# Optimization experiments

Measured on AMD Instinct MI355X. Metric: run time of the kernel, lower is better.

The kernel has to match this reference:

```python
import jax, jax.numpy as jnp
import numpy as np

N = 50000        # nodes
E = 1600000      # edges (avg degree 32)
F_IN = 512       # input features
HID = 8          # hidden per head (hardcoded in module)
HEADS = 8        # in_head (hardcoded in module)
CLS = 16         # num_classes
NEG_SLOPE = 0.2  # PyG GATConv default


def setup_inputs() -> dict:
    key = jax.random.key(0)
    ks = jax.random.split(key, 12)
    s = 0.05
    return {
        "x": jax.random.normal(ks[0], (N, F_IN), dtype=jnp.float32),
        "edge_index": jax.random.randint(ks[1], (2, E), 0, N, dtype=jnp.int64),
        "W1": jax.random.normal(ks[2], (F_IN, HEADS * HID), dtype=jnp.float32) * s,
        "att_src1": jax.random.normal(ks[3], (HEADS, HID), dtype=jnp.float32) * s,
        "att_dst1": jax.random.normal(ks[4], (HEADS, HID), dtype=jnp.float32) * s,
        "bias1": jax.random.normal(ks[5], (HEADS * HID,), dtype=jnp.float32) * s,
        "W2": jax.random.normal(ks[6], (HEADS * HID, CLS), dtype=jnp.float32) * s,
        "att_src2": jax.random.normal(ks[7], (1, CLS), dtype=jnp.float32) * s,
        "att_dst2": jax.random.normal(ks[8], (1, CLS), dtype=jnp.float32) * s,
        "bias2": jax.random.normal(ks[9], (CLS,), dtype=jnp.float32) * s,
    }


def _gat_conv(x, src, dst, W, att_src, att_dst, bias, n, heads, ch, concat):
    # Linear projection: [n, heads, ch]
    h = (x @ W).reshape(n, heads, ch)
    # Per-node attention logits (PyG style): alpha_src/dst = sum(h * a)
    a_src = jnp.einsum("nhc,hc->nh", h, att_src)  # [n, heads]
    a_dst = jnp.einsum("nhc,hc->nh", h, att_dst)
    # Per-edge raw score, leaky_relu, then segment softmax over incoming edges per dst
    e = jax.nn.leaky_relu(a_src[src] + a_dst[dst], NEG_SLOPE)  # [Etot, heads]
    m = jax.ops.segment_max(e, dst, num_segments=n)            # [n, heads]
    w = jnp.exp(e - m[dst])
    den = jax.ops.segment_sum(w, dst, num_segments=n)
    alpha = w / den[dst]                                        # [Etot, heads]
    # Scatter-aggregate weighted source features
    out = jax.ops.segment_sum(h[src] * alpha[..., None], dst, num_segments=n)  # [n, heads, ch]
    out = out.reshape(n, heads * ch) if concat else out.mean(axis=1)
    return out + bias


def reference(x, edge_index, W1, att_src1, att_dst1, bias1, W2, att_src2, att_dst2, bias2):
    n = x.shape[0]
    # PyG GATConv adds self-loops by default
    loops = jnp.arange(n, dtype=edge_index.dtype)
    src = jnp.concatenate([edge_index[0], loops])
    dst = jnp.concatenate([edge_index[1], loops])
    # dropout(p=0.6) is identity in eval mode
    h = _gat_conv(x, src, dst, W1, att_src1, att_dst1, bias1, n, HEADS, HID, True)
    h = jax.nn.elu(h)
    out = _gat_conv(h, src, dst, W2, att_src2, att_dst2, bias2, n, 1, CLS, False)
    return jax.nn.log_softmax(out, axis=1)
```

## Files before the change

### kernel.cpp

```cpp
#include <hip/hip_runtime.h>
#include <cstddef>

#define N_NODES 50000
#define N_EDGES 1600000
#define N_ETOT  (N_EDGES + N_NODES)
#define F_IN    512
#define HEADS   8
#define HID     8
#define CLS     16

#define NBUCK   196
#define BCAP    12288
#define CHUNKA  4096

typedef float v4 __attribute__((ext_vector_type(4)));
typedef float v2 __attribute__((ext_vector_type(2)));
typedef unsigned short us4 __attribute__((ext_vector_type(4)));
typedef unsigned int u4 __attribute__((ext_vector_type(4)));

__device__ inline float b2f_lo(unsigned int u) { return __uint_as_float(u << 16); }
__device__ inline float b2f_hi(unsigned int u) { return __uint_as_float(u & 0xffff0000u); }
__device__ inline unsigned short f2b(float f) {
  unsigned int x = __float_as_uint(f);
  unsigned int r = (x + 0x7fffu + ((x >> 16) & 1u)) >> 16;
  return (unsigned short)r;
}

__global__ __launch_bounds__(256) void gemm1_kernel(
    const float* __restrict__ x, const float* __restrict__ W,
    const float* __restrict__ att_src, const float* __restrict__ att_dst,
    unsigned short* __restrict__ h1b, float* __restrict__ a_src,
    float* __restrict__ a_dst, int nrows) {
  __shared__ float xs[64][36];
  __shared__ float ws[32][68];
  int t  = threadIdx.x;
  int tx = t & 15, ty = t >> 4;
  int row0 = blockIdx.x * 64;
  v4 acc[4];
  acc[0] = 0.f; acc[1] = 0.f; acc[2] = 0.f; acc[3] = 0.f;

  for (int k0 = 0; k0 < F_IN; k0 += 32) {
#pragma unroll
    for (int r = 0; r < 2; ++r) {
      int idx = t + r * 256;
      int m = idx >> 3;
      int kk = (idx & 7) * 4;
      v4 v = 0.f;
      int grow = row0 + m;
      if (grow < nrows) v = *(const v4*)(x + (size_t)grow * F_IN + k0 + kk);
      *(v4*)&xs[m][kk] = v;
    }
#pragma unroll
    for (int r = 0; r < 2; ++r) {
      int idx = t + r * 256;
      int kk = idx >> 4;
      int nn = (idx & 15) * 4;
      *(v4*)&ws[kk][nn] = *(const v4*)(W + (size_t)(k0 + kk) * 64 + nn);
    }
    __syncthreads();
#pragma unroll
    for (int kk = 0; kk < 32; kk += 4) {
      v4 a[4], b[4];
#pragma unroll
      for (int i = 0; i < 4; ++i) a[i] = *(const v4*)&xs[ty * 4 + i][kk];
#pragma unroll
      for (int tt = 0; tt < 4; ++tt) b[tt] = *(const v4*)&ws[kk + tt][tx * 4];
#pragma unroll
      for (int i = 0; i < 4; ++i) {
        acc[i] += a[i][0] * b[0];
        acc[i] += a[i][1] * b[1];
        acc[i] += a[i][2] * b[2];
        acc[i] += a[i][3] * b[3];
      }
    }
    __syncthreads();
  }
  v4 avs = *(const v4*)(att_src + tx * 4);
  v4 avd = *(const v4*)(att_dst + tx * 4);
#pragma unroll
  for (int i = 0; i < 4; ++i) {
    int grow = row0 + ty * 4 + i;
    float ps = acc[i][0]*avs[0] + acc[i][1]*avs[1] + acc[i][2]*avs[2] + acc[i][3]*avs[3];
    float pd = acc[i][0]*avd[0] + acc[i][1]*avd[1] + acc[i][2]*avd[2] + acc[i][3]*avd[3];
    ps += __shfl_xor(ps, 1);
    pd += __shfl_xor(pd, 1);
    if (grow < nrows) {
      us4 o;
      o.x = f2b(acc[i][0]); o.y = f2b(acc[i][1]);
      o.z = f2b(acc[i][2]); o.w = f2b(acc[i][3]);
      *(us4*)(h1b + (size_t)grow * 64 + tx * 4) = o;
      if (!(tx & 1)) {
        int head = tx >> 1;
        a_src[grow * 8 + head] = ps;
        a_dst[grow * 8 + head] = pd;
      }
    }
  }
}

__global__ __launch_bounds__(256) void bucketA_kernel(
    const int* __restrict__ src_idx, const int* __restrict__ dst_idx,
    int* __restrict__ gcur, int* __restrict__ abuck) {
  __shared__ int hist[NBUCK];
  __shared__ int base[NBUCK];
  __shared__ int cur[NBUCK];
  int t = threadIdx.x;
  if (t < NBUCK) hist[t] = 0;
  __syncthreads();
  int e0 = blockIdx.x * CHUNKA;
  int eend = e0 + CHUNKA;
  if (eend > N_EDGES) eend = N_EDGES;
  for (int e = e0 + t; e < eend; e += 256)
    atomicAdd(&hist[(unsigned)dst_idx[e] >> 8], 1);
  __syncthreads();
  if (t < NBUCK) {
    int c = hist[t];
    base[t] = c ? atomicAdd(&gcur[t], c) : 0;
    cur[t] = 0;
  }
  __syncthreads();
  for (int e = e0 + t; e < eend; e += 256) {
    int s = src_idx[e];
    int d = dst_idx[e];
    int b = (unsigned)d >> 8;
    int r = atomicAdd(&cur[b], 1);
    abuck[b * BCAP + base[b] + r] = (s << 8) | (d & 255);
  }
}

__global__ __launch_bounds__(256) void bucket_scan_kernel(
    const int* __restrict__ gcur, int* __restrict__ bucket_base,
    int* __restrict__ indptr) {
  __shared__ int sm[256];
  int t = threadIdx.x;
  int nnodes = N_NODES - t * 256;
  if (nnodes > 256) nnodes = 256;
  if (nnodes < 0) nnodes = 0;
  int v = (t < NBUCK) ? gcur[t] + nnodes : 0;
  sm[t] = v;
  __syncthreads();
  for (int o = 1; o < 256; o <<= 1) {
    int u = (t >= o) ? sm[t - o] : 0;
    __syncthreads();
    sm[t] += u;
    __syncthreads();
  }
  if (t < NBUCK) bucket_base[t] = sm[t] - v;
  if (t == 0) indptr[N_NODES] = N_ETOT;
}

__global__ __launch_bounds__(256) void bucketB_kernel(
    const int* __restrict__ gcur, const int* __restrict__ bucket_base,
    const int* __restrict__ abuck, int* __restrict__ indptr,
    int* __restrict__ csr_src) {
  __shared__ int hist[256];
  __shared__ int sm[256];
  __shared__ int cur[256];
  int b = blockIdx.x;
  int t = threadIdx.x;
  int M = gcur[b];
  int node0 = b * 256;
  int nnodes = N_NODES - node0;
  if (nnodes > 256) nnodes = 256;
  hist[t] = (t < nnodes) ? 1 : 0;
  __syncthreads();
  const int* ab = abuck + b * BCAP;
  for (int i = t; i < M; i += 256)
    atomicAdd(&hist[ab[i] & 255], 1);
  __syncthreads();
  int v = hist[t];
  sm[t] = v;
  __syncthreads();
  for (int o = 1; o < 256; o <<= 1) {
    int u = (t >= o) ? sm[t - o] : 0;
    __syncthreads();
    sm[t] += u;
    __syncthreads();
  }
  int bbase = bucket_base[b];
  int excl = sm[t] - v;
  cur[t] = excl;
  if (t < nnodes) indptr[node0 + t] = bbase + excl;
  __syncthreads();
  for (int i = t; i < M; i += 256) {
    int entry = ab[i];
    int r = atomicAdd(&cur[entry & 255], 1);
    csr_src[bbase + r] = entry >> 8;
  }
  if (t < nnodes) {
    int r = atomicAdd(&cur[t], 1);
    csr_src[bbase + r] = node0 + t;
  }
}

__global__ __launch_bounds__(256) void agg1_kernel(
    const int* __restrict__ indptr, const int* __restrict__ csr_src,
    const unsigned short* __restrict__ h1b, const float* __restrict__ a_src1,
    const float* __restrict__ a_dst1, const float* __restrict__ bias1,
    float* __restrict__ h_elu, int n) {
  int wave = threadIdx.x >> 6;
  int lane = threadIdx.x & 63;
  int node = blockIdx.x * 4 + wave;
  if (node >= n) return;
  int j = lane >> 3;
  int h = lane & 7;
  float adst = a_dst1[(unsigned)(node * 8 + h)];
  int beg = indptr[node], end = indptr[node + 1];
  float acc0=0.f, acc1=0.f, acc2=0.f, acc3=0.f, acc4=0.f, acc5=0.f, acc6=0.f, acc7=0.f;
  float den = 0.f;
  for (int base = beg; base < end; base += 64) {
    int m = end - base;
    if (m > 64) m = 64;
    int sv = (lane < m) ? csr_src[base + lane] : 0;
    for (int p = 0; p < m; p += 8) {
      int s = __shfl(sv, p + j);
      bool act = (p + j) < m;
      float e = a_src1[(unsigned)(s * 8 + h)] + adst;
      e = (e > 0.f) ? e : 0.2f * e;
      float w = act ? __expf(e) : 0.f;
      den += w;
      u4 f = *(const u4*)(h1b + (unsigned)(s * 64 + h * 8));
      acc0 += w * b2f_lo(f.x); acc1 += w * b2f_hi(f.x);
      acc2 += w * b2f_lo(f.y); acc3 += w * b2f_hi(f.y);
      acc4 += w * b2f_lo(f.z); acc5 += w * b2f_hi(f.z);
      acc6 += w * b2f_lo(f.w); acc7 += w * b2f_hi(f.w);
    }
  }
#pragma unroll
  for (int o = 8; o < 64; o <<= 1) {
    den  += __shfl_xor(den, o);
    acc0 += __shfl_xor(acc0, o); acc1 += __shfl_xor(acc1, o);
    acc2 += __shfl_xor(acc2, o); acc3 += __shfl_xor(acc3, o);
    acc4 += __shfl_xor(acc4, o); acc5 += __shfl_xor(acc5, o);
    acc6 += __shfl_xor(acc6, o); acc7 += __shfl_xor(acc7, o);
  }
  if (j == 0) {
    float inv = 1.f / den;
    v4 b0 = *(const v4*)(bias1 + h * 8);
    v4 b1 = *(const v4*)(bias1 + h * 8 + 4);
    v4 o0, o1;
    o0[0] = acc0 * inv + b0[0]; o0[1] = acc1 * inv + b0[1];
    o0[2] = acc2 * inv + b0[2]; o0[3] = acc3 * inv + b0[3];
    o1[0] = acc4 * inv + b1[0]; o1[1] = acc5 * inv + b1[1];
    o1[2] = acc6 * inv + b1[2]; o1[3] = acc7 * inv + b1[3];
#pragma unroll
    for (int k = 0; k < 4; ++k) {
      o0[k] = (o0[k] > 0.f) ? o0[k] : expm1f(o0[k]);
      o1[k] = (o1[k] > 0.f) ? o1[k] : expm1f(o1[k]);
    }
    *(v4*)(h_elu + (size_t)node * 64 + h * 8)     = o0;
    *(v4*)(h_elu + (size_t)node * 64 + h * 8 + 4) = o1;
  }
}

__global__ __launch_bounds__(256) void gemm2_kernel(
    const float* __restrict__ h_elu, const float* __restrict__ W2,
    const float* __restrict__ att_src2, const float* __restrict__ att_dst2,
    unsigned short* __restrict__ h2b, float* __restrict__ a_src2,
    float* __restrict__ a_dst2, int n) {
  __shared__ float xs[64][68];
  __shared__ float ws[64][16];
  int t = threadIdx.x;
  int row0 = blockIdx.x * 64;
  {
    int k = t >> 2, c4 = (t & 3) * 4;
    *(v4*)&ws[k][c4] = *(const v4*)(W2 + (size_t)k * 16 + c4);
  }
#pragma unroll
  for (int r = 0; r < 4; ++r) {
    int idx = t + r * 256;
    int m = idx >> 4;
    int c4 = (idx & 15) * 4;
    v4 v = 0.f;
    int grow = row0 + m;
    if (grow < n) v = *(const v4*)(h_elu + (size_t)grow * 64 + c4);
    *(v4*)&xs[m][c4] = v;
  }
  __syncthreads();
  int r = t >> 2, q = t & 3;
  int grow = row0 + r;
  v4 acc = 0.f;
#pragma unroll
  for (int k = 0; k < 64; ++k) {
    acc += xs[r][k] * *(const v4*)&ws[k][q * 4];
  }
  v4 asv = *(const v4*)(att_src2 + q * 4);
  v4 adv = *(const v4*)(att_dst2 + q * 4);
  float ps = acc[0] * asv[0] + acc[1] * asv[1] + acc[2] * asv[2] + acc[3] * asv[3];
  float pd = acc[0] * adv[0] + acc[1] * adv[1] + acc[2] * adv[2] + acc[3] * adv[3];
  ps += __shfl_xor(ps, 1); ps += __shfl_xor(ps, 2);
  pd += __shfl_xor(pd, 1); pd += __shfl_xor(pd, 2);
  if (grow < n) {
    us4 o;
    o.x = f2b(acc[0]); o.y = f2b(acc[1]); o.z = f2b(acc[2]); o.w = f2b(acc[3]);
    *(us4*)(h2b + (size_t)grow * 16 + q * 4) = o;
    if (q == 0) { a_src2[grow] = ps; a_dst2[grow] = pd; }
  }
}

__global__ __launch_bounds__(256) void agg2_kernel(
    const int* __restrict__ indptr, const int* __restrict__ csr_src,
    const unsigned short* __restrict__ h2b, const float* __restrict__ a_src2,
    const float* __restrict__ a_dst2, const float* __restrict__ bias2,
    float* __restrict__ out, int n) {
  int wave = threadIdx.x >> 6;
  int lane = threadIdx.x & 63;
  int node = blockIdx.x * 4 + wave;
  if (node >= n) return;
  int j = lane >> 3;
  int sub = lane & 7;
  float adst = a_dst2[node];
  int beg = indptr[node], end = indptr[node + 1];
  float acc0 = 0.f, acc1 = 0.f, den = 0.f;
  for (int base = beg; base < end; base += 64) {
    int m = end - base;
    if (m > 64) m = 64;
    int sv = (lane < m) ? csr_src[base + lane] : 0;
    for (int p = 0; p < m; p += 8) {
      int s = __shfl(sv, p + j);
      bool act = (p + j) < m;
      float e = a_src2[(unsigned)s] + adst;
      e = (e > 0.f) ? e : 0.2f * e;
      float w = act ? __expf(e) : 0.f;
      den += w;
      unsigned int f = *(const unsigned int*)(h2b + (unsigned)(s * 16 + sub * 2));
      acc0 += w * b2f_lo(f);
      acc1 += w * b2f_hi(f);
    }
  }
#pragma unroll
  for (int o = 8; o < 64; o <<= 1) {
    den  += __shfl_xor(den, o);
    acc0 += __shfl_xor(acc0, o);
    acc1 += __shfl_xor(acc1, o);
  }
  float inv = 1.f / den;
  float v0 = acc0 * inv + bias2[sub * 2];
  float v1 = acc1 * inv + bias2[sub * 2 + 1];
  float mx = fmaxf(v0, v1);
#pragma unroll
  for (int o = 1; o < 8; o <<= 1) mx = fmaxf(mx, __shfl_xor(mx, o));
  float ss = __expf(v0 - mx) + __expf(v1 - mx);
#pragma unroll
  for (int o = 1; o < 8; o <<= 1) ss += __shfl_xor(ss, o);
  float lg = mx + __logf(ss);
  if (j == 0) {
    v2 r;
    r[0] = v0 - lg;
    r[1] = v1 - lg;
    *(v2*)(out + (size_t)node * 16 + sub * 2) = r;
  }
}

extern "C" void kernel_launch(void* const* d_in, const int* in_sizes, int n_in,
                              void* d_out, int out_size, void* d_ws, size_t ws_size,
                              hipStream_t stream) {
  const float* x        = (const float*)d_in[0];
  const int*   ei       = (const int*)d_in[1];
  const float* W1       = (const float*)d_in[2];
  const float* att_src1 = (const float*)d_in[3];
  const float* att_dst1 = (const float*)d_in[4];
  const float* bias1    = (const float*)d_in[5];
  const float* W2       = (const float*)d_in[6];
  const float* att_src2 = (const float*)d_in[7];
  const float* att_dst2 = (const float*)d_in[8];
  const float* bias2    = (const float*)d_in[9];
  const int* src_idx = ei;
  const int* dst_idx = ei + N_EDGES;

  char* p = (char*)d_ws;
  auto alloc = [&](size_t bytes) {
    void* r = (void*)p;
    p += (bytes + 255) & ~(size_t)255;
    return r;
  };
  unsigned short* h1b = (unsigned short*)alloc((size_t)N_NODES * 64 * 2);
  float* h_elu   = (float*)alloc((size_t)N_NODES * 64 * 4);
  float* a_src1  = (float*)alloc((size_t)N_NODES * 8 * 4);
  float* a_dst1  = (float*)alloc((size_t)N_NODES * 8 * 4);
  unsigned short* h2b = (unsigned short*)alloc((size_t)N_NODES * 16 * 2);
  float* a_src2  = (float*)alloc((size_t)N_NODES * 4);
  float* a_dst2  = (float*)alloc((size_t)N_NODES * 4);
  int* indptr    = (int*)alloc((size_t)(N_NODES + 1) * 4);
  int* gcur      = (int*)alloc((size_t)NBUCK * 4);
  int* bucket_base = (int*)alloc((size_t)(NBUCK + 1) * 4);
  int* csr_src   = (int*)alloc((size_t)N_ETOT * 4);
  int* abuck     = (int*)h_elu;

  hipMemsetAsync(gcur, 0, (size_t)NBUCK * 4, stream);

  gemm1_kernel<<<(N_NODES + 63) / 64, 256, 0, stream>>>(
      x, W1, att_src1, att_dst1, h1b, a_src1, a_dst1, N_NODES);

  bucketA_kernel<<<(N_EDGES + CHUNKA - 1) / CHUNKA, 256, 0, stream>>>(
      src_idx, dst_idx, gcur, abuck);
  bucket_scan_kernel<<<1, 256, 0, stream>>>(gcur, bucket_base, indptr);
  bucketB_kernel<<<NBUCK, 256, 0, stream>>>(
      gcur, bucket_base, abuck, indptr, csr_src);

  agg1_kernel<<<N_NODES / 4, 256, 0, stream>>>(
      indptr, csr_src, h1b, a_src1, a_dst1, bias1, h_elu, N_NODES);

  gemm2_kernel<<<(N_NODES + 63) / 64, 256, 0, stream>>>(
      h_elu, W2, att_src2, att_dst2, h2b, a_src2, a_dst2, N_NODES);

  agg2_kernel<<<N_NODES / 4, 256, 0, stream>>>(
      indptr, csr_src, h2b, a_src2, a_dst2, bias2, (float*)d_out, N_NODES);
}
```

Measured before the change: 342.3 us.

## Use bf16 MFMA for first-layer projection GEMM with pre-transposed weights

The first-layer x@W1 GEMM moves from FP32 vector FMAs to bf16 MFMA 16x16x32 instructions. x is converted to bf16 as it is staged into shared memory, and a new small kernel transposes W1 to bf16. The epilogue is rewritten for the MFMA accumulator layout, computing the per-head attention logits with wider shuffle reductions. This reduces compute cost in a GEMM that reads 100MB of x and is largely memory-bound, at the price of bf16 input rounding and an extra kernel launch.

```diff
diff --git a/kernel.cpp b/kernel.cpp
--- a/kernel.cpp
+++ b/kernel.cpp
@@ -17,6 +17,8 @@
 typedef float v2 __attribute__((ext_vector_type(2)));
 typedef unsigned short us4 __attribute__((ext_vector_type(4)));
 typedef unsigned int u4 __attribute__((ext_vector_type(4)));
+typedef short bfrag __attribute__((ext_vector_type(8)));
+typedef float ffrag __attribute__((ext_vector_type(4)));
 
 __device__ inline float b2f_lo(unsigned int u) { return __uint_as_float(u << 16); }
 __device__ inline float b2f_hi(unsigned int u) { return __uint_as_float(u & 0xffff0000u); }
@@ -26,73 +28,99 @@
   return (unsigned short)r;
 }
 
+__global__ __launch_bounds__(256) void w1t_kernel(
+    const float* __restrict__ W, unsigned short* __restrict__ WT) {
+  int t = blockIdx.x * 256 + threadIdx.x;
+  if (t >= F_IN * 64) return;
+  int k = t >> 6, n = t & 63;
+  WT[n * F_IN + k] = f2b(W[t]);
+}
+
 __global__ __launch_bounds__(256) void gemm1_kernel(
-    const float* __restrict__ x, const float* __restrict__ W,
+    const float* __restrict__ x, const unsigned short* __restrict__ W1bT,
     const float* __restrict__ att_src, const float* __restrict__ att_dst,
     unsigned short* __restrict__ h1b, float* __restrict__ a_src,
     float* __restrict__ a_dst, int nrows) {
-  __shared__ float xs[64][36];
-  __shared__ float ws[32][68];
-  int t  = threadIdx.x;
-  int tx = t & 15, ty = t >> 4;
+  __shared__ unsigned short xsb[64][72];
+  __shared__ unsigned short wsb[64][72];
+  int t = threadIdx.x;
+  int lane = t & 63;
+  int w = t >> 6;
   int row0 = blockIdx.x * 64;
-  v4 acc[4];
+  ffrag acc[4];
   acc[0] = 0.f; acc[1] = 0.f; acc[2] = 0.f; acc[3] = 0.f;
 
-  for (int k0 = 0; k0 < F_IN; k0 += 32) {
-#pragma unroll
-    for (int r = 0; r < 2; ++r) {
-      int idx = t + r * 256;
-      int m = idx >> 3;
-      int kk = (idx & 7) * 4;
+  int mrow = lane & 15;
+  int koff = (lane >> 4) * 8;
+
+  for (int kt = 0; kt < 8; ++kt) {
+    int k0 = kt * 64;
+#pragma unroll
+    for (int r = 0; r < 4; ++r) {
+      int slot = t + r * 256;
+      int m = slot >> 4;
+      int k4 = (slot & 15) * 4;
       v4 v = 0.f;
       int grow = row0 + m;
-      if (grow < nrows) v = *(const v4*)(x + (size_t)grow * F_IN + k0 + kk);
-      *(v4*)&xs[m][kk] = v;
+      if (grow < nrows) v = *(const v4*)(x + (size_t)grow * F_IN + k0 + k4);
+      us4 o;
+      o.x = f2b(v[0]); o.y = f2b(v[1]); o.z = f2b(v[2]); o.w = f2b(v[3]);
+      *(us4*)&xsb[m][k4] = o;
     }
 #pragma unroll
     for (int r = 0; r < 2; ++r) {
-      int idx = t + r * 256;
-      int kk = idx >> 4;
-      int nn = (idx & 15) * 4;
-      *(v4*)&ws[kk][nn] = *(const v4*)(W + (size_t)(k0 + kk) * 64 + nn);
-    }
-    __syncthreads();
-#pragma unroll
-    for (int kk = 0; kk < 32; kk += 4) {
-      v4 a[4], b[4];
-#pragma unroll
-      for (int i = 0; i < 4; ++i) a[i] = *(const v4*)&xs[ty * 4 + i][kk];
-#pragma unroll
-      for (int tt = 0; tt < 4; ++tt) b[tt] = *(const v4*)&ws[kk + tt][tx * 4];
-#pragma unroll
-      for (int i = 0; i < 4; ++i) {
-        acc[i] += a[i][0] * b[0];
-        acc[i] += a[i][1] * b[1];
-        acc[i] += a[i][2] * b[2];
-        acc[i] += a[i][3] * b[3];
+      int slot = t + r * 256;
+      int nn = slot >> 3;
+      int k8 = (slot & 7) * 8;
+      *(bfrag*)&wsb[nn][k8] = *(const bfrag*)(W1bT + nn * F_IN + k0 + k8);
+    }
+    __syncthreads();
+#pragma unroll
+    for (int kk = 0; kk < 64; kk += 32) {
+      bfrag a = *(const bfrag*)&xsb[w * 16 + mrow][kk + koff];
+#pragma unroll
+      for (int tt = 0; tt < 4; ++tt) {
+        bfrag b = *(const bfrag*)&wsb[tt * 16 + mrow][kk + koff];
+        acc[tt] = __builtin_amdgcn_mfma_f32_16x16x32_bf16(a, b, acc[tt], 0, 0, 0);
       }
     }
     __syncthreads();
   }
-  v4 avs = *(const v4*)(att_src + tx * 4);
-  v4 avd = *(const v4*)(att_dst + tx * 4);
-#pragma unroll
-  for (int i = 0; i < 4; ++i) {
-    int grow = row0 + ty * 4 + i;
-    float ps = acc[i][0]*avs[0] + acc[i][1]*avs[1] + acc[i][2]*avs[2] + acc[i][3]*avs[3];
-    float pd = acc[i][0]*avd[0] + acc[i][1]*avd[1] + acc[i][2]*avd[2] + acc[i][3]*avd[3];
-    ps += __shfl_xor(ps, 1);
-    pd += __shfl_xor(pd, 1);
+  int c = lane & 15, q = lane >> 4;
+  float as_[4], ad_[4];
+#pragma unroll
+  for (int tt = 0; tt < 4; ++tt) {
+    as_[tt] = att_src[tt * 16 + c];
+    ad_[tt] = att_dst[tt * 16 + c];
+  }
+#pragma unroll
+  for (int r = 0; r < 4; ++r) {
+    int grow = row0 + w * 16 + q * 4 + r;
+    float ps[4], pd[4];
+#pragma unroll
+    for (int tt = 0; tt < 4; ++tt) {
+      ps[tt] = acc[tt][r] * as_[tt];
+      pd[tt] = acc[tt][r] * ad_[tt];
+    }
+#pragma unroll
+    for (int o = 1; o < 8; o <<= 1) {
+#pragma unroll
+      for (int tt = 0; tt < 4; ++tt) {
+        ps[tt] += __shfl_xor(ps[tt], o);
+        pd[tt] += __shfl_xor(pd[tt], o);
+      }
+    }
     if (grow < nrows) {
-      us4 o;
-      o.x = f2b(acc[i][0]); o.y = f2b(acc[i][1]);
-      o.z = f2b(acc[i][2]); o.w = f2b(acc[i][3]);
-      *(us4*)(h1b + (size_t)grow * 64 + tx * 4) = o;
-      if (!(tx & 1)) {
-        int head = tx >> 1;
-        a_src[grow * 8 + head] = ps;
-        a_dst[grow * 8 + head] = pd;
+#pragma unroll
+      for (int tt = 0; tt < 4; ++tt)
+        h1b[(size_t)grow * 64 + tt * 16 + c] = f2b(acc[tt][r]);
+      if ((c & 7) == 0) {
+#pragma unroll
+        for (int tt = 0; tt < 4; ++tt) {
+          int head = tt * 2 + (c >> 3);
+          a_src[grow * 8 + head] = ps[tt];
+          a_dst[grow * 8 + head] = pd[tt];
+        }
       }
     }
   }
@@ -385,12 +413,14 @@
   int* gcur      = (int*)alloc((size_t)NBUCK * 4);
   int* bucket_base = (int*)alloc((size_t)(NBUCK + 1) * 4);
   int* csr_src   = (int*)alloc((size_t)N_ETOT * 4);
+  unsigned short* W1bT = (unsigned short*)alloc((size_t)64 * F_IN * 2);
   int* abuck     = (int*)h_elu;
 
   hipMemsetAsync(gcur, 0, (size_t)NBUCK * 4, stream);
 
+  w1t_kernel<<<(F_IN * 64 + 255) / 256, 256, 0, stream>>>(W1, W1bT);
   gemm1_kernel<<<(N_NODES + 63) / 64, 256, 0, stream>>>(
-      x, W1, att_src1, att_dst1, h1b, a_src1, a_dst1, N_NODES);
+      x, W1bT, att_src1, att_dst1, h1b, a_src1, a_dst1, N_NODES);
 
   bucketA_kernel<<<(N_EDGES + CHUNKA - 1) / CHUNKA, 256, 0, stream>>>(
       src_idx, dst_idx, gcur, abuck);
```

After: 323.8 us. -5.4%, faster.
